# Kernel optimization log

Hardware: AMD Instinct MI355X
Metric: run time of the kernel (lower is better)

The kernel has to match this reference:

```python
import jax, jax.numpy as jnp
import numpy as np
import math

# Model dims (from init_kwargs)
BATCH, SEQ, D_MODEL = 2, 1024, 1024
D_STATE, D_CONV, EXPAND = 16, 4, 2
D_INNER = EXPAND * D_MODEL          # 2048
DT_RANK = math.ceil(D_MODEL / 16)   # 64
DT_MIN, DT_MAX, DT_FLOOR = 1e-3, 1e-1, 1e-4


def setup_inputs() -> dict:
    key = jax.random.key(0)
    ks = jax.random.split(key, 9)
    x = jax.random.normal(ks[0], (BATCH, SEQ, D_MODEL), dtype=jnp.float32)
    # Dense kernels are (in, out) as in keras
    W_in = jax.random.normal(ks[1], (D_MODEL, 2 * D_INNER), jnp.float32) / np.sqrt(D_MODEL)
    conv_k = jax.random.normal(ks[2], (D_CONV, 1, D_INNER), jnp.float32) * 0.2  # depthwise (W, I/g=1, O)
    conv_b = jnp.zeros((D_INNER,), jnp.float32)
    W_x = jax.random.normal(ks[3], (D_INNER, DT_RANK + 2 * D_STATE), jnp.float32) / np.sqrt(D_INNER)
    dt_init_std = DT_RANK ** -0.5
    W_dt = jax.random.uniform(ks[4], (DT_RANK, D_INNER), jnp.float32, -dt_init_std, dt_init_std)
    dt = jnp.exp(jax.random.uniform(ks[5], (D_INNER,), jnp.float32)
                 * (math.log(DT_MAX) - math.log(DT_MIN)) + math.log(DT_MIN))
    dt = jnp.clip(dt, DT_FLOOR, None)
    b_dt = jnp.log(jnp.expm1(dt))  # inverse softplus
    W_out = jax.random.normal(ks[6], (D_INNER, D_MODEL), jnp.float32) / np.sqrt(D_INNER)
    # S4D-real init: A_log = log([1..d_state]) per channel
    A_log = jnp.log(jnp.tile(jnp.arange(1, D_STATE + 1, dtype=jnp.float32), (D_INNER, 1)))
    D = jnp.ones((D_INNER,), jnp.float32)
    return {"x": x, "W_in": W_in, "conv_k": conv_k, "conv_b": conv_b, "W_x": W_x,
            "W_dt": W_dt, "b_dt": b_dt, "W_out": W_out, "A_log": A_log, "D": D}


def reference(x, W_in, conv_k, conv_b, W_x, W_dt, b_dt, W_out, A_log, D):
    # Input projection and split into SSM path (u) and gate (z)
    xz = x @ W_in                                   # (B, L, 2*d_inner)
    u, z = jnp.split(xz, 2, axis=-1)                # each (B, L, d_inner)
    # Causal depthwise conv1d
    u = jax.lax.conv_general_dilated(
        u, conv_k, window_strides=(1,), padding=[(D_CONV - 1, 0)],
        dimension_numbers=("NWC", "WIO", "NWC"), feature_group_count=D_INNER) + conv_b
    u = jax.nn.silu(u)
    # Data-dependent SSM parameters
    x_dbl = u @ W_x                                 # (B, L, dt_rank + 2*d_state)
    dt_lo, Bm, Cm = jnp.split(x_dbl, [DT_RANK, DT_RANK + D_STATE], axis=-1)
    delta = jax.nn.softplus(dt_lo @ W_dt + b_dt)    # (B, L, d_inner)
    A = -jnp.exp(A_log)                             # (d_inner, d_state)
    # Discretize: A_bar = exp(delta*A), B_bar*u = delta*u outer B
    dA = jnp.exp(delta[..., None] * A)                       # (B, L, d_inner, d_state)
    dBu = (delta * u)[..., None] * Bm[:, :, None, :]         # (B, L, d_inner, d_state)

    def step(h, inp):
        dA_t, dBu_t, C_t = inp                      # (B,d,n), (B,d,n), (B,n)
        h = dA_t * h + dBu_t
        y = jnp.einsum("bdn,bn->bd", h, C_t)
        return h, y

    h0 = jnp.zeros((BATCH, D_INNER, D_STATE), x.dtype)
    _, ys = jax.lax.scan(step, h0, (jnp.swapaxes(dA, 0, 1),
                                    jnp.swapaxes(dBu, 0, 1),
                                    jnp.swapaxes(Cm, 0, 1)))
    y = jnp.swapaxes(ys, 0, 1) + u * D              # skip connection
    y = y * jax.nn.silu(z)                          # gating
    return y @ W_out                                # (B, L, d_model)
```

## Files before the change

kernel.cpp:

```cpp
#include <hip/hip_runtime.h>
#include <hip/hip_bf16.h>
#include <math.h>

typedef __hip_bfloat16 bf16;
typedef __bf16 bf16x8 __attribute__((ext_vector_type(8)));
typedef float floatx4 __attribute__((ext_vector_type(4)));

#define LOG2E 1.44269504088896340736f
#define DINNER 2048
#define NCHUNK 32
#define CLEN 32

static __device__ __forceinline__ void gl_lds16(const void* g, void* l) {
  __builtin_amdgcn_global_load_lds(
      (const __attribute__((address_space(1))) void*)g,
      (__attribute__((address_space(3))) void*)l, 16, 0, 0);
}

static __device__ __forceinline__ void tr32(const float* __restrict__ src,
                                            bf16* __restrict__ dst, int R, int C,
                                            int tile, bf16 (*t)[33]) {
  int ctiles = C >> 5;
  int c0 = (tile % ctiles) << 5, r0 = (tile / ctiles) << 5;
  int tx = threadIdx.x & 31, ty = threadIdx.x >> 5;
#pragma unroll
  for (int i = 0; i < 4; i++)
    t[ty + i * 8][tx] = __float2bfloat16(src[(size_t)(r0 + ty + i * 8) * C + c0 + tx]);
  __syncthreads();
#pragma unroll
  for (int i = 0; i < 4; i++)
    dst[(size_t)(c0 + ty + i * 8) * R + r0 + tx] = t[tx][ty + i * 8];
}

__global__ void prep1(const float* __restrict__ W_in, const float* __restrict__ W_x,
                      const float* __restrict__ W_dt, const float* __restrict__ W_out,
                      const float* __restrict__ x,
                      bf16* __restrict__ WinT, bf16* __restrict__ WxT,
                      bf16* __restrict__ WdtT, bf16* __restrict__ WoutT,
                      bf16* __restrict__ xb) {
  __shared__ bf16 t[32][33];
  int b = blockIdx.x;
  if (b < 4096) { tr32(W_in, WinT, 1024, 4096, b, t); return; }
  b -= 4096;
  if (b < 192)  { tr32(W_x, WxT, 2048, 96, b, t); return; }
  b -= 192;
  if (b < 128)  { tr32(W_dt, WdtT, 64, 2048, b, t); return; }
  b -= 128;
  if (b < 2048) { tr32(W_out, WoutT, 2048, 1024, b, t); return; }
  b -= 2048;
  int base = b * 2048 + threadIdx.x;
#pragma unroll
  for (int i = 0; i < 8; i++)
    xb[base + i * 256] = __float2bfloat16(x[base + i * 256]);
}

__global__ __launch_bounds__(256, 4)
void gemm128(const bf16* __restrict__ A, const bf16* __restrict__ Bt,
             int M, int N, int K, int lda, int ldb, int ksplit,
             float* __restrict__ outF, bf16* __restrict__ outB,
             const float* __restrict__ bias, int flags) {
  __shared__ char smem[24576];
  bf16* As = (bf16*)smem;
  bf16* Bs = (bf16*)(smem + 16384);
  const int tid = threadIdx.x;
  const int wave = tid >> 6, lane = tid & 63;
  const int wm = wave & 1, wn = wave >> 1;
  const int m0 = blockIdx.y * 128, n0 = blockIdx.x * 64;
  const int kper = K / ksplit;
  const int kbeg = blockIdx.z * kper, kend = kbeg + kper;

  floatx4 acc[4][2];
#pragma unroll
  for (int i = 0; i < 4; i++)
#pragma unroll
    for (int j = 0; j < 2; j++) acc[i][j] = (floatx4){0.f, 0.f, 0.f, 0.f};

  const int fr = lane & 15, quad = lane >> 4;
  const int lrow = lane >> 3;
  const int slot = lane & 7;
  const int kcol = (slot ^ lrow) * 8;

  for (int k0 = kbeg; k0 < kend; k0 += 64) {
    __syncthreads();
#pragma unroll
    for (int g = 0; g < 4; g++) {
      int grp = wave * 4 + g;
      int ra = m0 + grp * 8 + lrow;
      gl_lds16(A + (size_t)ra * lda + k0 + kcol, (char*)As + grp * 1024 + lane * 16);
    }
#pragma unroll
    for (int g = 0; g < 2; g++) {
      int grp = wave * 2 + g;
      int rb = n0 + grp * 8 + lrow; if (rb > N - 1) rb = N - 1;
      gl_lds16(Bt + (size_t)rb * ldb + k0 + kcol, (char*)Bs + grp * 1024 + lane * 16);
    }
    __syncthreads();
#pragma unroll
    for (int ks = 0; ks < 2; ks++) {
      bf16x8 af[4], bfr[2];
#pragma unroll
      for (int i = 0; i < 4; i++) {
        int row = wm * 64 + i * 16 + fr;
        af[i] = *reinterpret_cast<const bf16x8*>(&As[row * 64 + (((ks * 4 + quad) ^ (row & 7)) * 8)]);
      }
#pragma unroll
      for (int j = 0; j < 2; j++) {
        int row = wn * 32 + j * 16 + fr;
        bfr[j] = *reinterpret_cast<const bf16x8*>(&Bs[row * 64 + (((ks * 4 + quad) ^ (row & 7)) * 8)]);
      }
#pragma unroll
      for (int i = 0; i < 4; i++)
#pragma unroll
        for (int j = 0; j < 2; j++)
          acc[i][j] = __builtin_amdgcn_mfma_f32_16x16x32_bf16(af[i], bfr[j], acc[i][j], 0, 0, 0);
    }
  }

  if (outB) {
    __syncthreads();
    bf16* Cs = (bf16*)smem;
#pragma unroll
    for (int i = 0; i < 4; i++)
#pragma unroll
      for (int j = 0; j < 2; j++) {
        int col = wn * 32 + j * 16 + fr;
        float b = bias ? bias[n0 + col] : 0.f;
#pragma unroll
        for (int r = 0; r < 4; r++) {
          int row = wm * 64 + i * 16 + quad * 4 + r;
          float v = acc[i][j][r] + b;
          if (flags & 1) v = fmaxf(v, 0.f) + __logf(1.f + __expf(-fabsf(v)));
          Cs[row * 72 + col] = __float2bfloat16(v);
        }
      }
    __syncthreads();
#pragma unroll
    for (int it = 0; it < 4; it++) {
      int e = it * 256 + tid;
      int row = e >> 3, col = (e & 7) * 8;
      *reinterpret_cast<float4*>(&outB[(size_t)(m0 + row) * N + n0 + col]) =
          *reinterpret_cast<const float4*>(&Cs[row * 72 + col]);
    }
    return;
  }
#pragma unroll
  for (int i = 0; i < 4; i++) {
#pragma unroll
    for (int j = 0; j < 2; j++) {
      int col = n0 + wn * 32 + j * 16 + fr;
      if (col >= N) continue;
#pragma unroll
      for (int r = 0; r < 4; r++) {
        int row = m0 + wm * 64 + i * 16 + quad * 4 + r;
        float v = acc[i][j][r];
        if (flags & 8) {
          outF[(size_t)blockIdx.z * M * N + (size_t)row * N + col] = v;
        } else {
          if (bias) v += bias[col];
          if (flags & 1) v = fmaxf(v, 0.f) + __logf(1.f + __expf(-fabsf(v)));
          outF[(size_t)row * N + col] = v;
        }
      }
    }
  }
}

__global__ void conv_silu(const bf16* __restrict__ xzb, const float* __restrict__ ck,
                          const float* __restrict__ cb, bf16* __restrict__ u) {
  int d = blockIdx.x * 256 + threadIdx.x;
  int r0 = blockIdx.y * 8;
  int t0 = r0 & 1023;
  float k0 = ck[0 * DINNER + d];
  float k1 = ck[1 * DINNER + d];
  float k2 = ck[2 * DINNER + d];
  float k3 = ck[3 * DINNER + d];
  float bias = cb[d];
  float in[11];
#pragma unroll
  for (int i = 0; i < 11; i++) {
    int t = t0 - 3 + i;
    in[i] = (t >= 0) ? __bfloat162float(xzb[(size_t)(r0 - 3 + i) * 4096 + d]) : 0.f;
  }
#pragma unroll
  for (int i = 0; i < 8; i++) {
    float v = bias + in[i] * k0 + in[i + 1] * k1 + in[i + 2] * k2 + in[i + 3] * k3;
    v = v / (1.f + __expf(-v));
    u[(size_t)(r0 + i) * DINNER + d] = __float2bfloat16(v);
  }
}

__global__ void reduce_xdbl(const float* __restrict__ pb, float* __restrict__ xdbl,
                            bf16* __restrict__ dt) {
  int g = blockIdx.x * 256 + threadIdx.x;
  float s = 0.f;
#pragma unroll
  for (int z = 0; z < 8; z++) s += pb[(size_t)z * 2048 * 96 + g];
  xdbl[g] = s;
  int r = g / 96, j = g - r * 96;
  if (j < 64) dt[r * 64 + j] = __float2bfloat16(s);
}

__global__ void reduce_out(const float* __restrict__ pb, float* __restrict__ out) {
  int g = blockIdx.x * 256 + threadIdx.x;
  const int S = 2048 * 1024;
  out[g] = (pb[g] + pb[S + g]) + (pb[2 * S + g] + pb[3 * S + g]);
}

__global__ void scanA(const bf16* __restrict__ delta, const bf16* __restrict__ u,
                      const float* __restrict__ xdbl, const float* __restrict__ A_log,
                      float* __restrict__ hend, float* __restrict__ Ssum) {
  int d = blockIdx.x * 256 + threadIdx.x;
  int c = blockIdx.y, b = blockIdx.z;
  float al2e[16];
#pragma unroll
  for (int n = 0; n < 16; n++)
    al2e[n] = -__expf(A_log[d * 16 + n]) * LOG2E;
  float h[16];
#pragma unroll
  for (int n = 0; n < 16; n++) h[n] = 0.f;
  float S = 0.f;
  int t0 = c * CLEN;
  for (int t = t0; t < t0 + CLEN; ++t) {
    int r = b * 1024 + t;
    float dt = __bfloat162float(delta[(size_t)r * DINNER + d]);
    float ut = __bfloat162float(u[(size_t)r * DINNER + d]);
    float du = dt * ut;
    S += dt;
    const float* bc = xdbl + (size_t)r * 96 + 64;
#pragma unroll
    for (int n = 0; n < 16; n++) {
      float dA = exp2f(dt * al2e[n]);
      h[n] = dA * h[n] + du * bc[n];
    }
  }
  size_t base = (((size_t)(b * NCHUNK + c) * DINNER) + d) * 16;
#pragma unroll
  for (int n = 0; n < 16; n++) hend[base + n] = h[n];
  Ssum[(b * NCHUNK + c) * DINNER + d] = S;
}

__global__ void scanB(float* __restrict__ hend, const float* __restrict__ Ssum,
                      const float* __restrict__ A_log) {
  int g = blockIdx.x * 256 + threadIdx.x;
  int n = g & 15, d = (g >> 4) & 2047, b = g >> 15;
  float al2e = -__expf(A_log[d * 16 + n]) * LOG2E;
  float H = 0.f;
#pragma unroll
  for (int c = 0; c < NCHUNK; c++) {
    size_t idx = (((size_t)(b * NCHUNK + c) * DINNER) + d) * 16 + n;
    float he = hend[idx];
    float P = exp2f(Ssum[(b * NCHUNK + c) * DINNER + d] * al2e);
    hend[idx] = H;
    H = P * H + he;
  }
}

__global__ void scanC(const bf16* __restrict__ delta, const bf16* __restrict__ u,
                      const float* __restrict__ xdbl, const bf16* __restrict__ xzb,
                      const float* __restrict__ A_log, const float* __restrict__ Dv,
                      const float* __restrict__ Hin, bf16* __restrict__ yg) {
  int d = blockIdx.x * 256 + threadIdx.x;
  int c = blockIdx.y, b = blockIdx.z;
  float al2e[16];
#pragma unroll
  for (int n = 0; n < 16; n++)
    al2e[n] = -__expf(A_log[d * 16 + n]) * LOG2E;
  float Dd = Dv[d];
  float h[16];
  size_t hb = (((size_t)(b * NCHUNK + c) * DINNER) + d) * 16;
#pragma unroll
  for (int n = 0; n < 16; n++) h[n] = Hin[hb + n];
  int t0 = c * CLEN;
  for (int t = t0; t < t0 + CLEN; ++t) {
    int r = b * 1024 + t;
    float dt = __bfloat162float(delta[(size_t)r * DINNER + d]);
    float ut = __bfloat162float(u[(size_t)r * DINNER + d]);
    float du = dt * ut;
    float z = __bfloat162float(xzb[(size_t)r * 4096 + 2048 + d]);
    const float* bc = xdbl + (size_t)r * 96 + 64;
    float y = 0.f;
#pragma unroll
    for (int n = 0; n < 16; n++) {
      float dA = exp2f(dt * al2e[n]);
      h[n] = dA * h[n] + du * bc[n];
      y += h[n] * bc[16 + n];
    }
    y += ut * Dd;
    y *= z / (1.f + __expf(-z));
    yg[(size_t)r * 4096 + d] = __float2bfloat16(y);
  }
}

extern "C" void kernel_launch(void* const* d_in, const int* in_sizes, int n_in,
                              void* d_out, int out_size, void* d_ws, size_t ws_size,
                              hipStream_t stream) {
  const float* x     = (const float*)d_in[0];
  const float* W_in  = (const float*)d_in[1];
  const float* ck    = (const float*)d_in[2];
  const float* cb    = (const float*)d_in[3];
  const float* W_x   = (const float*)d_in[4];
  const float* W_dt  = (const float*)d_in[5];
  const float* b_dt  = (const float*)d_in[6];
  const float* W_out = (const float*)d_in[7];
  const float* A_log = (const float*)d_in[8];
  const float* Dv    = (const float*)d_in[9];
  float* out = (float*)d_out;
  (void)in_sizes; (void)n_in; (void)out_size; (void)ws_size;

  char* w = (char*)d_ws;
  size_t off = 0;
  auto alloc = [&](size_t nb) { void* p = w + off; off += (nb + 255) & ~(size_t)255; return p; };

  bf16*  WinT  = (bf16*) alloc((size_t)4096 * 1024 * 2);
  bf16*  WxT   = (bf16*) alloc((size_t)96 * 2048 * 2);
  bf16*  WdtT  = (bf16*) alloc((size_t)2048 * 64 * 2);
  bf16*  WoutT = (bf16*) alloc((size_t)1024 * 2048 * 2);
  bf16*  xb    = (bf16*) alloc((size_t)2048 * 1024 * 2);
  bf16*  xzb   = (bf16*) alloc((size_t)2048 * 4096 * 2);
  bf16*  u     = (bf16*) alloc((size_t)2048 * 2048 * 2);
  float* xdbl  = (float*)alloc((size_t)2048 * 96 * 4);
  bf16*  dt    = (bf16*) alloc((size_t)2048 * 64 * 2);
  float* hend  = (float*)alloc((size_t)2 * NCHUNK * 2048 * 16 * 4);
  float* Ssum  = (float*)alloc((size_t)2 * NCHUNK * 2048 * 4);
  float* pb4   = (float*)alloc((size_t)4 * 2048 * 1024 * 4);

  bf16*  delta = WinT;
  bf16*  yg    = xzb;
  float* pb2   = hend;

  prep1<<<7488, 256, 0, stream>>>(W_in, W_x, W_dt, W_out, x, WinT, WxT, WdtT, WoutT, xb);
  gemm128<<<dim3(64, 16, 1), 256, 0, stream>>>(xb, WinT, 2048, 4096, 1024, 1024, 1024, 1,
                                               nullptr, xzb, nullptr, 0);
  conv_silu<<<dim3(8, 256), 256, 0, stream>>>(xzb, ck, cb, u);
  gemm128<<<dim3(2, 16, 8), 256, 0, stream>>>(u, WxT, 2048, 96, 2048, 2048, 2048, 8,
                                              pb2, nullptr, nullptr, 8);
  reduce_xdbl<<<768, 256, 0, stream>>>(pb2, xdbl, dt);
  gemm128<<<dim3(32, 16, 1), 256, 0, stream>>>(dt, WdtT, 2048, 2048, 64, 64, 64, 1,
                                               nullptr, delta, b_dt, 1);
  scanA<<<dim3(8, NCHUNK, 2), 256, 0, stream>>>(delta, u, xdbl, A_log, hend, Ssum);
  scanB<<<256, 256, 0, stream>>>(hend, Ssum, A_log);
  scanC<<<dim3(8, NCHUNK, 2), 256, 0, stream>>>(delta, u, xdbl, xzb, A_log, Dv, hend, yg);
  gemm128<<<dim3(16, 16, 4), 256, 0, stream>>>(yg, WoutT, 2048, 1024, 2048, 4096, 2048, 4,
                                               pb4, nullptr, nullptr, 8);
  reduce_out<<<8192, 256, 0, stream>>>(pb4, out);
}
```

Measured before the change: 237.1 us.

## Use atomic split-K output, dedicated dt GEMM kernel, vectorized x conversion

The output projection now accumulates its split-K partials into the output with atomicAdd after a memset. This removes the 32 MB partial buffer and the separate reduce_out kernel. A specialised 64x64 single-tile kernel handles the K=64 dt projection with fused bias and softplus, replacing the generic 128-row GEMM. The x-to-bf16 conversion in prep1 now uses float4 vector loads and stores. Atomics make the output summation order nondeterministic and add contention on the output.

```diff
diff --git a/kernel.cpp b/kernel.cpp
--- a/kernel.cpp
+++ b/kernel.cpp
@@ -15,6 +15,10 @@
   __builtin_amdgcn_global_load_lds(
       (const __attribute__((address_space(1))) void*)g,
       (__attribute__((address_space(3))) void*)l, 16, 0, 0);
+}
+
+static __device__ __forceinline__ float softplus_f(float v) {
+  return fmaxf(v, 0.f) + __logf(1.f + __expf(-fabsf(v)));
 }
 
 static __device__ __forceinline__ void tr32(const float* __restrict__ src,
@@ -48,10 +52,14 @@
   b -= 128;
   if (b < 2048) { tr32(W_out, WoutT, 2048, 1024, b, t); return; }
   b -= 2048;
-  int base = b * 2048 + threadIdx.x;
-#pragma unroll
-  for (int i = 0; i < 8; i++)
-    xb[base + i * 256] = __float2bfloat16(x[base + i * 256]);
+  int base = b * 2048 + threadIdx.x * 8;
+  float4 a = *reinterpret_cast<const float4*>(&x[base]);
+  float4 c = *reinterpret_cast<const float4*>(&x[base + 4]);
+  bf16 o[8] = {__float2bfloat16(a.x), __float2bfloat16(a.y),
+               __float2bfloat16(a.z), __float2bfloat16(a.w),
+               __float2bfloat16(c.x), __float2bfloat16(c.y),
+               __float2bfloat16(c.z), __float2bfloat16(c.w)};
+  *reinterpret_cast<float4*>(&xb[base]) = *reinterpret_cast<const float4*>(o);
 }
 
 __global__ __launch_bounds__(256, 4)
@@ -128,9 +136,7 @@
 #pragma unroll
         for (int r = 0; r < 4; r++) {
           int row = wm * 64 + i * 16 + quad * 4 + r;
-          float v = acc[i][j][r] + b;
-          if (flags & 1) v = fmaxf(v, 0.f) + __logf(1.f + __expf(-fabsf(v)));
-          Cs[row * 72 + col] = __float2bfloat16(v);
+          Cs[row * 72 + col] = __float2bfloat16(acc[i][j][r] + b);
         }
       }
     __syncthreads();
@@ -153,15 +159,80 @@
       for (int r = 0; r < 4; r++) {
         int row = m0 + wm * 64 + i * 16 + quad * 4 + r;
         float v = acc[i][j][r];
-        if (flags & 8) {
-          outF[(size_t)blockIdx.z * M * N + (size_t)row * N + col] = v;
-        } else {
-          if (bias) v += bias[col];
-          if (flags & 1) v = fmaxf(v, 0.f) + __logf(1.f + __expf(-fabsf(v)));
-          outF[(size_t)row * N + col] = v;
-        }
+        if (flags & 16)     atomicAdd(&outF[(size_t)row * N + col], v);
+        else if (flags & 8) outF[(size_t)blockIdx.z * M * N + (size_t)row * N + col] = v;
+        else                outF[(size_t)row * N + col] = v;
       }
     }
+  }
+}
+
+__global__ __launch_bounds__(256, 4)
+void gemm_dt(const bf16* __restrict__ A, const bf16* __restrict__ Bt,
+             const float* __restrict__ bias, bf16* __restrict__ outB) {
+  __shared__ bf16 smem[2][64 * 64];
+  bf16* As = smem[0]; bf16* Bs = smem[1];
+  const int tid = threadIdx.x, wave = tid >> 6, lane = tid & 63;
+  const int wm = wave & 1, wn = wave >> 1;
+  const int m0 = blockIdx.x * 64, n0 = blockIdx.y * 64;
+  const int fr = lane & 15, quad = lane >> 4;
+  const int lrow = lane >> 3, slot = lane & 7;
+  const int kcol = (slot ^ lrow) * 8;
+
+#pragma unroll
+  for (int g = 0; g < 2; g++) {
+    int grp = wave * 2 + g;
+    gl_lds16(A + (size_t)(m0 + grp * 8 + lrow) * 64 + kcol, (char*)As + grp * 1024 + lane * 16);
+    gl_lds16(Bt + (size_t)(n0 + grp * 8 + lrow) * 64 + kcol, (char*)Bs + grp * 1024 + lane * 16);
+  }
+  __syncthreads();
+
+  floatx4 acc[2][2];
+#pragma unroll
+  for (int i = 0; i < 2; i++)
+#pragma unroll
+    for (int j = 0; j < 2; j++) acc[i][j] = (floatx4){0.f, 0.f, 0.f, 0.f};
+#pragma unroll
+  for (int ks = 0; ks < 2; ks++) {
+    bf16x8 af[2], bfr[2];
+#pragma unroll
+    for (int i = 0; i < 2; i++) {
+      int row = wm * 32 + i * 16 + fr;
+      af[i] = *reinterpret_cast<const bf16x8*>(&As[row * 64 + (((ks * 4 + quad) ^ (row & 7)) * 8)]);
+    }
+#pragma unroll
+    for (int j = 0; j < 2; j++) {
+      int row = wn * 32 + j * 16 + fr;
+      bfr[j] = *reinterpret_cast<const bf16x8*>(&Bs[row * 64 + (((ks * 4 + quad) ^ (row & 7)) * 8)]);
+    }
+#pragma unroll
+    for (int i = 0; i < 2; i++)
+#pragma unroll
+      for (int j = 0; j < 2; j++)
+        acc[i][j] = __builtin_amdgcn_mfma_f32_16x16x32_bf16(af[i], bfr[j], acc[i][j], 0, 0, 0);
+  }
+
+  __syncthreads();
+  bf16* Cs = smem[0];
+#pragma unroll
+  for (int i = 0; i < 2; i++)
+#pragma unroll
+    for (int j = 0; j < 2; j++) {
+      int col = wn * 32 + j * 16 + fr;
+      float b = bias[n0 + col];
+#pragma unroll
+      for (int r = 0; r < 4; r++) {
+        int row = wm * 32 + i * 16 + quad * 4 + r;
+        Cs[row * 72 + col] = __float2bfloat16(softplus_f(acc[i][j][r] + b));
+      }
+    }
+  __syncthreads();
+#pragma unroll
+  for (int it = 0; it < 2; it++) {
+    int e = it * 256 + tid;
+    int row = e >> 3, col = (e & 7) * 8;
+    *reinterpret_cast<float4*>(&outB[(size_t)(m0 + row) * 2048 + n0 + col]) =
+        *reinterpret_cast<const float4*>(&Cs[row * 72 + col]);
   }
 }
 
@@ -198,12 +269,6 @@
   xdbl[g] = s;
   int r = g / 96, j = g - r * 96;
   if (j < 64) dt[r * 64 + j] = __float2bfloat16(s);
-}
-
-__global__ void reduce_out(const float* __restrict__ pb, float* __restrict__ out) {
-  int g = blockIdx.x * 256 + threadIdx.x;
-  const int S = 2048 * 1024;
-  out[g] = (pb[g] + pb[S + g]) + (pb[2 * S + g] + pb[3 * S + g]);
 }
 
 __global__ void scanA(const bf16* __restrict__ delta, const bf16* __restrict__ u,
@@ -322,12 +387,12 @@
   bf16*  dt    = (bf16*) alloc((size_t)2048 * 64 * 2);
   float* hend  = (float*)alloc((size_t)2 * NCHUNK * 2048 * 16 * 4);
   float* Ssum  = (float*)alloc((size_t)2 * NCHUNK * 2048 * 4);
-  float* pb4   = (float*)alloc((size_t)4 * 2048 * 1024 * 4);
 
   bf16*  delta = WinT;
   bf16*  yg    = xzb;
   float* pb2   = hend;
 
+  hipMemsetAsync(out, 0, (size_t)2048 * 1024 * 4, stream);
   prep1<<<7488, 256, 0, stream>>>(W_in, W_x, W_dt, W_out, x, WinT, WxT, WdtT, WoutT, xb);
   gemm128<<<dim3(64, 16, 1), 256, 0, stream>>>(xb, WinT, 2048, 4096, 1024, 1024, 1024, 1,
                                                nullptr, xzb, nullptr, 0);
@@ -335,12 +400,10 @@
   gemm128<<<dim3(2, 16, 8), 256, 0, stream>>>(u, WxT, 2048, 96, 2048, 2048, 2048, 8,
                                               pb2, nullptr, nullptr, 8);
   reduce_xdbl<<<768, 256, 0, stream>>>(pb2, xdbl, dt);
-  gemm128<<<dim3(32, 16, 1), 256, 0, stream>>>(dt, WdtT, 2048, 2048, 64, 64, 64, 1,
-                                               nullptr, delta, b_dt, 1);
+  gemm_dt<<<dim3(32, 32), 256, 0, stream>>>(dt, WdtT, b_dt, delta);
   scanA<<<dim3(8, NCHUNK, 2), 256, 0, stream>>>(delta, u, xdbl, A_log, hend, Ssum);
   scanB<<<256, 256, 0, stream>>>(hend, Ssum, A_log);
   scanC<<<dim3(8, NCHUNK, 2), 256, 0, stream>>>(delta, u, xdbl, xzb, A_log, Dv, hend, yg);
   gemm128<<<dim3(16, 16, 4), 256, 0, stream>>>(yg, WoutT, 2048, 1024, 2048, 4096, 2048, 4,
-                                               pb4, nullptr, nullptr, 8);
-  reduce_out<<<8192, 256, 0, stream>>>(pb4, out);
-}
+                                               out, nullptr, nullptr, 16);
+}
```

Measured after the change: 239.7 us. About the same (+1.1%).
